# Optimization experiments

Hardware: AMD Instinct MI355X
Metric: run time of the kernel (lower is better)

The kernel has to match this reference:

```python
import jax, jax.numpy as jnp
import numpy as np

N_NODES = 307
U = 100          # gru units / GAT out dim
D_IN = 3         # per-node input features
F_IN = U + D_IN  # 103, GATv2 input dim
NEG_SLOPE = 0.2


def setup_inputs() -> dict:
    key = jax.random.key(0)
    ks = jax.random.split(key, 12)
    B, E = 256, 4096
    inputs = jax.random.normal(ks[0], (B, N_NODES * D_IN), dtype=jnp.float32)
    state = jax.random.normal(ks[1], (B, N_NODES * U), dtype=jnp.float32)
    src = jax.random.randint(ks[2], (E,), 0, N_NODES, dtype=jnp.int32)
    dst = jax.random.randint(ks[3], (E,), 0, N_NODES, dtype=jnp.int32)
    def glorot(k, shape):
        lim = float(np.sqrt(6.0 / (shape[0] + shape[1])))
        return jax.random.uniform(k, shape, jnp.float32, -lim, lim)
    return {
        "inputs": inputs, "state": state, "src": src, "dst": dst,
        "Wl": glorot(ks[4], (F_IN, U)),        # GATv2 lin_l (source)
        "Wr": glorot(ks[5], (F_IN, U)),        # GATv2 lin_r (target)
        "att": jax.random.normal(ks[6], (U,), jnp.float32) * 0.1,
        "gat_bias": jnp.zeros((U,), jnp.float32),
        "bias_gc": jnp.zeros((U,), jnp.float32),   # self.bias_1 added in _gc3
        "W_gru1": glorot(ks[7], (F_IN, 2 * U)),    # GRULinear(100,200)
        "b_gru1": jnp.zeros((2 * U,), jnp.float32),
        "W_gru2": glorot(ks[8], (F_IN, U)),        # GRULinear(100,100)
        "b_gru2": jnp.zeros((U,), jnp.float32),
    }


def _gru_linear(inputs, hidden, W, b):
    # cat((inputs[B,N,3], hidden[B,N,U]), -1) @ W + b
    B = hidden.shape[0]
    x = jnp.concatenate([inputs.reshape(B, N_NODES, D_IN),
                         hidden.reshape(B, N_NODES, U)], axis=2)
    return jnp.einsum('bnf,fo->bno', x, W) + b


def _gatv2(x, src, dst, Wl, Wr, att, gat_bias):
    # x: (B, N, F_IN); PyG GATv2Conv with heads=1, add_self_loops=True
    loops = jnp.arange(N_NODES, dtype=src.dtype)
    s = jnp.concatenate([src, loops])
    d = jnp.concatenate([dst, loops])
    xl = jnp.einsum('bnf,fu->bnu', x, Wl)  # source transform
    xr = jnp.einsum('bnf,fu->bnu', x, Wr)  # target transform

    def per_sample(xl_b, xr_b):
        m = xl_b[s]                                        # (E', U)
        e = jax.nn.leaky_relu(m + xr_b[d], NEG_SLOPE) @ att  # (E',)
        emax = jax.ops.segment_max(e, d, num_segments=N_NODES)
        ex = jnp.exp(e - emax[d])
        denom = jax.ops.segment_sum(ex, d, num_segments=N_NODES)
        alpha = ex / denom[d]
        return jax.ops.segment_sum(alpha[:, None] * m, d, num_segments=N_NODES)

    out = jax.vmap(per_sample)(xl, xr)  # (B, N, U)
    return out + gat_bias


def reference(inputs, state, src, dst, Wl, Wr, att, gat_bias, bias_gc,
              W_gru1, b_gru1, W_gru2, b_gru2):
    B = state.shape[0]
    # _gc3: cat([state, inputs]) -> GATv2 per sample -> + bias_1
    x = jnp.concatenate([state.reshape(B, N_NODES, U),
                         inputs.reshape(B, N_NODES, D_IN)], axis=2)
    st = _gatv2(x, src, dst, Wl, Wr, att, gat_bias) + bias_gc
    st = st.reshape(B, N_NODES * U)
    # GRU gating
    value = jax.nn.sigmoid(_gru_linear(inputs, st, W_gru1, b_gru1))  # (B,N,2U)
    r, u = jnp.split(value, 2, axis=-1)
    r = r.reshape(B, N_NODES * U)
    u = u.reshape(B, N_NODES * U)
    c = jnp.tanh(_gru_linear(inputs, r * st, W_gru2, b_gru2)).reshape(B, N_NODES * U)
    return u * st + (1.0 - u) * c
```

## Files before the change

kernel.cpp:

```cpp
#include <hip/hip_runtime.h>
#include <math.h>

#define NN 307
#define UU 100
#define DD 3
#define UP 104
#define UNIT_W 14336
#define SC_CAP 4608
#define EI_CAP 4416
#define NTILE 20
#define NT 512

typedef _Float16 f16;
typedef f16  f16x2 __attribute__((ext_vector_type(2)));
typedef f16  f16x4 __attribute__((ext_vector_type(4)));
typedef f16  f16x8 __attribute__((ext_vector_type(8)));
typedef float f32x4 __attribute__((ext_vector_type(4)));
typedef unsigned short u16;

__global__ __launch_bounds__(256)
void pack_w_k(const float* __restrict__ Wl, const float* __restrict__ Wr,
              const float* __restrict__ Wg1, const float* __restrict__ Wg2,
              f16* __restrict__ Wp)
{
    const int idx = blockIdx.x * 256 + threadIdx.x;
    const int u   = idx / UNIT_W;
    const int rem = idx - u * UNIT_W;
    const int e   = rem & 7;
    const int l   = (rem >> 3) & 63;
    const int sj  = rem >> 9;
    const int s   = sj / 7, j = sj - 7 * s;
    const int col = j * 16 + (l & 15);
    const int k   = (s * 4 + (l >> 4)) * 8 + e;
    float v = 0.f;
    if (col < UU && k < UU + DD) {
        if (u == 0)      v = Wl[k * UU + col];
        else if (u == 1) v = Wr[k * UU + col];
        else {
            const int kk = (k < UU) ? (k + DD) : (k - UU);
            if (u == 2)      v = Wg1[kk * (2 * UU) + col];
            else if (u == 3) v = Wg1[kk * (2 * UU) + UU + col];
            else             v = Wg2[kk * UU + col];
        }
    }
    Wp[idx] = (f16)v;
}

__global__ __launch_bounds__(64)
void csr_count_k(const int* __restrict__ dst, int E, int* offs)
{
    const int d = blockIdx.x;
    const int lane = threadIdx.x;
    const int Etot = E + NN;
    int c = 0;
    for (int base = 0; base < Etot; base += 64) {
        const int e = base + lane;
        if (e < Etot) {
            const int de = (e < E) ? dst[e] : (e - E);
            c += (de == d) ? 1 : 0;
        }
    }
    #pragma unroll
    for (int m = 1; m < 64; m <<= 1) c += __shfl_xor(c, m, 64);
    if (lane == 0) {
        offs[d + 1] = c;
        if (d == 0) offs[0] = 0;
    }
}

__global__ __launch_bounds__(512)
void csr_scan_k(int* offs)
{
    __shared__ int c[512];
    const int t = threadIdx.x;
    c[t] = (t < NN) ? offs[t + 1] : 0;
    __syncthreads();
    #pragma unroll
    for (int off = 1; off < 512; off <<= 1) {
        const int v = (t >= off) ? c[t - off] : 0;
        __syncthreads();
        c[t] += v;
        __syncthreads();
    }
    if (t < NN) offs[t + 1] = c[t];
    if (t == 0) offs[0] = 0;
}

__global__ __launch_bounds__(64)
void csr_fill_k(const int* __restrict__ src, const int* __restrict__ dst,
                int E, const int* __restrict__ offs,
                int* eidx, int* ddst)
{
    const int d = blockIdx.x;
    const int lane = threadIdx.x;
    const int Etot = E + NN;
    int w = offs[d];
    for (int base = 0; base < Etot; base += 64) {
        const int e = base + lane;
        bool match = false;
        int se = 0;
        if (e < Etot) {
            const int de = (e < E) ? dst[e] : (e - E);
            se           = (e < E) ? src[e] : (e - E);
            match = (de == d);
        }
        const unsigned long long mask = __ballot(match);
        if (match) {
            const int pos = w + __popcll(mask & ((1ULL << lane) - 1ULL));
            eidx[pos] = se;
            ddst[pos] = d;
        }
        w += __popcll(mask);
    }
}

__device__ __forceinline__ void mma_unit1(const f16x8 (&af)[4],
                                          const f16* __restrict__ Wu,
                                          int l, f32x4 (&acc)[7])
{
    #pragma unroll
    for (int s = 0; s < 4; ++s) {
        #pragma unroll
        for (int j = 0; j < 7; ++j) {
            const f16x8 bv = *(const f16x8*)(Wu + (((s * 7 + j) * 64 + l) << 3));
            acc[j] = __builtin_amdgcn_mfma_f32_16x16x32_f16(af[s], bv, acc[j], 0, 0, 0);
        }
        __builtin_amdgcn_sched_barrier(0);
    }
}

__device__ __forceinline__ void z7(f32x4 (&acc)[7])
{
    #pragma unroll
    for (int j = 0; j < 7; ++j) acc[j] = (f32x4)0.f;
}

__global__ __launch_bounds__(NT)
__attribute__((amdgpu_waves_per_eu(2)))
void gat_all_k(const float* __restrict__ state, const float* __restrict__ inputs,
               const f16* __restrict__ Wp, const float* __restrict__ att,
               const float* __restrict__ gb, const float* __restrict__ bgc,
               const int* __restrict__ offs, const int* __restrict__ eidx,
               const int* __restrict__ ddst, int Etot,
               f16* __restrict__ stg)
{
    __shared__ f16   xl_s[NN * UP];
    __shared__ f16   xr_s[NN * UP];
    __shared__ float sc_s[SC_CAP];
    __shared__ u16   ei_s[EI_CAP];
    __shared__ f16   att_s[UP];

    const int b   = blockIdx.x;
    const int tid = threadIdx.x;
    const int w = tid >> 6, l = tid & 63, lr = l & 15, lk = l >> 4;
    const float* stf = state  + (size_t)b * NN * UU;
    const float* inb = inputs + (size_t)b * NN * DD;
    f16* stb = stg + (size_t)b * NN * UP;

    for (int q = tid; q < Etot; q += NT) ei_s[q] = (u16)eidx[q];
    for (int q = tid; q < 2 * NN; q += NT) {
        const int rr = (q < NN) ? q : (q - NN);
        f16* p = (q < NN) ? xl_s : xr_s;
        *(f16x4*)&p[rr * UP + 100] = (f16x4)(f16)0.f;
    }
    if (tid < UP) att_s[tid] = (tid < UU) ? (f16)att[tid] : (f16)0.f;

    for (int tile = w; tile < NTILE; tile += 8) {
        const int row  = tile * 16 + lr;
        const int crow = (row < NN) ? row : (NN - 1);
        const float* bf = stf + (size_t)crow * UU;
        f16x8 af[4];
        #pragma unroll
        for (int s = 0; s < 3; ++s) {
            const int kb = s * 4 + lk;
            const float4 x0 = *(const float4*)(bf + kb * 8);
            const float4 x1 = *(const float4*)(bf + kb * 8 + 4);
            f16x8 v;
            v[0]=(f16)x0.x; v[1]=(f16)x0.y; v[2]=(f16)x0.z; v[3]=(f16)x0.w;
            v[4]=(f16)x1.x; v[5]=(f16)x1.y; v[6]=(f16)x1.z; v[7]=(f16)x1.w;
            af[s] = v;
        }
        {
            f16x8 v = (f16x8)(f16)0.f;
            if (lk == 0) {
                const float4 x0 = *(const float4*)(bf + 96);
                v[0]=(f16)x0.x; v[1]=(f16)x0.y; v[2]=(f16)x0.z; v[3]=(f16)x0.w;
                v[4] = (f16)inb[(size_t)crow * DD + 0];
                v[5] = (f16)inb[(size_t)crow * DD + 1];
                v[6] = (f16)inb[(size_t)crow * DD + 2];
                v[7] = (f16)0.f;
            }
            af[3] = v;
        }
        __builtin_amdgcn_sched_barrier(0);
        #pragma unroll
        for (int u = 0; u < 2; ++u) {
            f32x4 acc[7];
            z7(acc);
            mma_unit1(af, Wp + (size_t)u * UNIT_W, l, acc);
            f16* dst = u ? xr_s : xl_s;
            #pragma unroll
            for (int j = 0; j < 7; ++j) {
                const int col = j * 16 + lr;
                if (col >= UU) continue;
                #pragma unroll
                for (int r = 0; r < 4; ++r) {
                    const int grow = tile * 16 + lk * 4 + r;
                    if (grow < NN) dst[grow * UP + col] = (f16)acc[j][r];
                }
            }
        }
    }
    __syncthreads();

    for (int i = tid; i < Etot; i += NT) {
        const int s = ei_s[i];
        const int d = ddst[i];
        const f16x8* a8 = (const f16x8*)&xl_s[s * UP];
        const f16x8* r8 = (const f16x8*)&xr_s[d * UP];
        float p0 = 0.f, p1 = 0.f;
        #pragma clang loop unroll(disable)
        for (int c = 0; c < 13; ++c) {
            const f16x8 x  = a8[c] + r8[c];
            const f16x8 xm = x * (f16)0.2f;
            const f16x8 y  = __builtin_elementwise_max(x, xm);
            const f16x2* y2  = (const f16x2*)&y;
            const f16x2* at2 = (const f16x2*)&att_s[c * 8];
#if __has_builtin(__builtin_amdgcn_fdot2)
            p0 = __builtin_amdgcn_fdot2(y2[0], at2[0], p0, false);
            p1 = __builtin_amdgcn_fdot2(y2[1], at2[1], p1, false);
            p0 = __builtin_amdgcn_fdot2(y2[2], at2[2], p0, false);
            p1 = __builtin_amdgcn_fdot2(y2[3], at2[3], p1, false);
#else
            #pragma unroll
            for (int q = 0; q < 4; ++q) {
                p0 += (float)y2[q][0] * (float)at2[q][0];
                p1 += (float)y2[q][1] * (float)at2[q][1];
            }
#endif
        }
        sc_s[i] = p0 + p1;
    }
    __syncthreads();

    if (tid < NN) {
        const int e0 = offs[tid], e1 = offs[tid + 1];
        float mx = -1e30f;
        for (int e = e0; e < e1; ++e) mx = fmaxf(mx, sc_s[e]);
        float dn = 0.f;
        for (int e = e0; e < e1; ++e) {
            const float ex = __expf(sc_s[e] - mx);
            sc_s[e] = ex;
            dn += ex;
        }
        const float inv = 1.f / dn;
        for (int e = e0; e < e1; ++e) sc_s[e] *= inv;
    }
    __syncthreads();

    {
        const int g   = tid >> 4;
        const int sub = tid & 15;
        const bool fa = (sub < 13);
        float bias_r[8];
        #pragma unroll
        for (int k = 0; k < 8; ++k) {
            const int f = sub * 8 + k;
            bias_r[k] = (fa && f < UU) ? (gb[f] + bgc[f]) : 0.f;
        }
        for (int d = g; d < NN; d += 32) {
            const int e0 = offs[d], e1 = offs[d + 1];
            float acc[8] = {0.f, 0.f, 0.f, 0.f, 0.f, 0.f, 0.f, 0.f};
            for (int e = e0; e < e1; ++e) {
                const float alpha = sc_s[e];
                const int s = ei_s[e];
                if (fa) {
                    const f16x8 m = *(const f16x8*)&xl_s[s * UP + sub * 8];
                    #pragma unroll
                    for (int k = 0; k < 8; ++k) acc[k] += alpha * (float)m[k];
                }
            }
            if (fa) {
                f16x8 o;
                #pragma unroll
                for (int k = 0; k < 8; ++k) o[k] = (f16)(acc[k] + bias_r[k]);
                *(f16x8*)(stb + (size_t)d * UP + sub * 8) = o;
            }
        }
    }
}

__global__ __launch_bounds__(256, 4)
void gru3_k(const f16* __restrict__ st, const float* __restrict__ inp,
            const f16* __restrict__ Wp2 ,
            const float* __restrict__ bg1, const float* __restrict__ bg2,
            float* __restrict__ out, int M)
{
    __shared__ f16 st_s[64 * UP];
    __shared__ f16 rst_s[64 * UP];

    const int tid = threadIdx.x;
    const int w = tid >> 6, l = tid & 63, lr = l & 15, lk = l >> 4;
    const int rb = blockIdx.x * 64 + w * 16;
    const int lbase = w * 16;

    #pragma unroll
    for (int p = 0; p < 4; ++p) {
        const int idx = p * 64 + l;
        const int row = idx >> 4, ch = idx & 15;
        if (ch < 13) {
            int gr = rb + row; if (gr >= M) gr = M - 1;
            *(f16x8*)&st_s[(lbase + row) * UP + ch * 8] =
                *(const f16x8*)(st + (size_t)gr * UP + ch * 8);
        }
    }

    int crow = rb + lr; if (crow >= M) crow = M - 1;
    const f16* bh = &st_s[(lbase + lr) * UP];
    f16x8 af[4];
    #pragma unroll
    for (int s = 0; s < 3; ++s)
        af[s] = *(const f16x8*)(bh + (s * 4 + lk) * 8);
    {
        f16x8 v = (f16x8)(f16)0.f;
        if (lk == 0) {
            v = *(const f16x8*)(bh + 96);
            v[4] = (f16)inp[(size_t)crow * DD + 0];
            v[5] = (f16)inp[(size_t)crow * DD + 1];
            v[6] = (f16)inp[(size_t)crow * DD + 2];
            v[7] = (f16)0.f;
        }
        af[3] = v;
    }
    __builtin_amdgcn_sched_barrier(0);

    f32x4 acc[7];

    z7(acc);
    mma_unit1(af, Wp2, l, acc);
    #pragma unroll
    for (int j = 0; j < 7; ++j) {
        const int col = j * 16 + lr;
        if (col >= UU) continue;
        const float bR = bg1[col];
        #pragma unroll
        for (int r = 0; r < 4; ++r) {
            const int grow = rb + lk * 4 + r;
            const int lrow = lbase + lk * 4 + r;
            if (grow < M) {
                const float stv = (float)st_s[lrow * UP + col];
                const float sg = 1.f / (1.f + __expf(-(acc[j][r] + bR)));
                rst_s[lrow * UP + col] = (f16)(sg * stv);
            }
        }
    }
    if (l < 16) {
        const int grow2 = rb + l;
        const int lrow2 = lbase + l;
        if (grow2 < M) {
            rst_s[lrow2 * UP + 100] = (f16)inp[(size_t)grow2 * DD + 0];
            rst_s[lrow2 * UP + 101] = (f16)inp[(size_t)grow2 * DD + 1];
            rst_s[lrow2 * UP + 102] = (f16)inp[(size_t)grow2 * DD + 2];
            rst_s[lrow2 * UP + 103] = (f16)0.f;
        }
    }
    __builtin_amdgcn_sched_barrier(0);

    z7(acc);
    mma_unit1(af, Wp2 + UNIT_W, l, acc);
    f16x4 uh[7];
    #pragma unroll
    for (int j = 0; j < 7; ++j) {
        const int col = j * 16 + lr;
        const float bU = (col < UU) ? bg1[UU + col] : 0.f;
        #pragma unroll
        for (int r = 0; r < 4; ++r)
            uh[j][r] = (f16)(1.f / (1.f + __expf(-(acc[j][r] + bU))));
    }

    f16x8 af2[4];
    #pragma unroll
    for (int s = 0; s < 3; ++s)
        af2[s] = *(const f16x8*)&rst_s[(lbase + lr) * UP + (s * 4 + lk) * 8];
    af2[3] = (lk == 0) ? *(const f16x8*)&rst_s[(lbase + lr) * UP + 96]
                       : (f16x8)(f16)0.f;
    __builtin_amdgcn_sched_barrier(0);

    z7(acc);
    mma_unit1(af2, Wp2 + 2 * UNIT_W, l, acc);
    #pragma unroll
    for (int j = 0; j < 7; ++j) {
        const int col = j * 16 + lr;
        if (col >= UU) continue;
        const float bC = bg2[col];
        #pragma unroll
        for (int r = 0; r < 4; ++r) {
            const int grow = rb + lk * 4 + r;
            const int lrow = lbase + lk * 4 + r;
            if (grow < M) {
                const float c = tanhf(acc[j][r] + bC);
                const float u = (float)uh[j][r];
                const float stv = (float)st_s[lrow * UP + col];
                out[(size_t)grow * UU + col] = u * stv + (1.f - u) * c;
            }
        }
    }
}

extern "C" void kernel_launch(void* const* d_in, const int* in_sizes, int n_in,
                              void* d_out, int out_size, void* d_ws, size_t ws_size,
                              hipStream_t stream)
{
    const float* inputs   = (const float*)d_in[0];
    const float* state    = (const float*)d_in[1];
    const int*   src      = (const int*)  d_in[2];
    const int*   dst      = (const int*)  d_in[3];
    const float* Wl       = (const float*)d_in[4];
    const float* Wr       = (const float*)d_in[5];
    const float* att      = (const float*)d_in[6];
    const float* gat_bias = (const float*)d_in[7];
    const float* bias_gc  = (const float*)d_in[8];
    const float* Wg1      = (const float*)d_in[9];
    const float* bg1      = (const float*)d_in[10];
    const float* Wg2      = (const float*)d_in[11];
    const float* bg2      = (const float*)d_in[12];

    const int E = in_sizes[2];
    const int B = in_sizes[1] / (NN * UU);
    const int M = B * NN;
    const int Etot = E + NN;

    char* ws = (char*)d_ws;
    f16* Wp   = (f16*)ws;
    int* offs = (int*)(ws + 5 * UNIT_W * sizeof(f16));
    int* eidx = offs + (NN + 1);
    int* ddst = eidx + (Etot + 64);
    f16* st_h = (f16*)(ws + (256 << 10));
    float* out = (float*)d_out;

    pack_w_k<<<280, 256, 0, stream>>>(Wl, Wr, Wg1, Wg2, Wp);
    csr_count_k<<<NN, 64, 0, stream>>>(dst, E, offs);
    csr_scan_k<<<1, 512, 0, stream>>>(offs);
    csr_fill_k<<<NN, 64, 0, stream>>>(src, dst, E, offs, eidx, ddst);

    gat_all_k<<<B, NT, 0, stream>>>(state, inputs, Wp, att,
        gat_bias, bias_gc, offs, eidx, ddst, Etot, st_h);

    gru3_k<<<(M + 63) / 64, 256, 0, stream>>>(st_h, inputs,
        Wp + 2 * (size_t)UNIT_W, bg1, bg2, out, M);
}
```

Baseline: 165.0 us.

## Split GAT into separate xl/xr GEMM kernel and lighter-LDS attention kernel

Moves the per-sample xl/xr projection GEMM out of the fused GAT kernel into its own batched GEMM kernel that writes fp16 xl/xr to workspace. The attention kernel then keeps only xl in shared memory, reads xr from global, and packs each edge's source index with an fp16 score/alpha into one 32-bit word. The goal is to cut LDS use so more blocks fit per CU, and to run the GEMM over the whole batch with better occupancy. In exchange it adds an extra global round-trip of xl/xr and stores scores and alphas in fp16, which lowers precision.

```diff
diff --git a/kernel.cpp b/kernel.cpp
--- a/kernel.cpp
+++ b/kernel.cpp
@@ -6,9 +6,7 @@
 #define DD 3
 #define UP 104
 #define UNIT_W 14336
-#define SC_CAP 4608
-#define EI_CAP 4416
-#define NTILE 20
+#define SE_CAP 4416
 #define NT 512
 
 typedef _Float16 f16;
@@ -17,6 +15,9 @@
 typedef f16  f16x8 __attribute__((ext_vector_type(8)));
 typedef float f32x4 __attribute__((ext_vector_type(4)));
 typedef unsigned short u16;
+
+__device__ __forceinline__ u16 f16_bits(f16 v) { u16 r; __builtin_memcpy(&r, &v, 2); return r; }
+__device__ __forceinline__ f16 bits_f16(u16 v) { f16 r; __builtin_memcpy(&r, &v, 2); return r; }
 
 __global__ __launch_bounds__(256)
 void pack_w_k(const float* __restrict__ Wl, const float* __restrict__ Wr,
@@ -135,40 +136,19 @@
     for (int j = 0; j < 7; ++j) acc[j] = (f32x4)0.f;
 }
 
-__global__ __launch_bounds__(NT)
-__attribute__((amdgpu_waves_per_eu(2)))
-void gat_all_k(const float* __restrict__ state, const float* __restrict__ inputs,
-               const f16* __restrict__ Wp, const float* __restrict__ att,
-               const float* __restrict__ gb, const float* __restrict__ bgc,
-               const int* __restrict__ offs, const int* __restrict__ eidx,
-               const int* __restrict__ ddst, int Etot,
-               f16* __restrict__ stg)
-{
-    __shared__ f16   xl_s[NN * UP];
-    __shared__ f16   xr_s[NN * UP];
-    __shared__ float sc_s[SC_CAP];
-    __shared__ u16   ei_s[EI_CAP];
-    __shared__ f16   att_s[UP];
-
-    const int b   = blockIdx.x;
+__global__ __launch_bounds__(256, 4)
+void gemm_xlxr_k(const float* __restrict__ state, const float* __restrict__ inp,
+                 const f16* __restrict__ Wp,
+                 f16* __restrict__ xl, f16* __restrict__ xr, int M)
+{
     const int tid = threadIdx.x;
     const int w = tid >> 6, l = tid & 63, lr = l & 15, lk = l >> 4;
-    const float* stf = state  + (size_t)b * NN * UU;
-    const float* inb = inputs + (size_t)b * NN * DD;
-    f16* stb = stg + (size_t)b * NN * UP;
-
-    for (int q = tid; q < Etot; q += NT) ei_s[q] = (u16)eidx[q];
-    for (int q = tid; q < 2 * NN; q += NT) {
-        const int rr = (q < NN) ? q : (q - NN);
-        f16* p = (q < NN) ? xl_s : xr_s;
-        *(f16x4*)&p[rr * UP + 100] = (f16x4)(f16)0.f;
-    }
-    if (tid < UP) att_s[tid] = (tid < UU) ? (f16)att[tid] : (f16)0.f;
-
-    for (int tile = w; tile < NTILE; tile += 8) {
-        const int row  = tile * 16 + lr;
-        const int crow = (row < NN) ? row : (NN - 1);
-        const float* bf = stf + (size_t)crow * UU;
+
+    #pragma clang loop unroll(disable)
+    for (int t = 0; t < 2; ++t) {
+        const int rb = blockIdx.x * 128 + w * 32 + t * 16;
+        int crow = rb + lr; if (crow >= M) crow = M - 1;
+        const float* bf = state + (size_t)crow * UU;
         f16x8 af[4];
         #pragma unroll
         for (int s = 0; s < 3; ++s) {
@@ -185,9 +165,9 @@
             if (lk == 0) {
                 const float4 x0 = *(const float4*)(bf + 96);
                 v[0]=(f16)x0.x; v[1]=(f16)x0.y; v[2]=(f16)x0.z; v[3]=(f16)x0.w;
-                v[4] = (f16)inb[(size_t)crow * DD + 0];
-                v[5] = (f16)inb[(size_t)crow * DD + 1];
-                v[6] = (f16)inb[(size_t)crow * DD + 2];
+                v[4] = (f16)inp[(size_t)crow * DD + 0];
+                v[5] = (f16)inp[(size_t)crow * DD + 1];
+                v[6] = (f16)inp[(size_t)crow * DD + 2];
                 v[7] = (f16)0.f;
             }
             af[3] = v;
@@ -198,26 +178,49 @@
             f32x4 acc[7];
             z7(acc);
             mma_unit1(af, Wp + (size_t)u * UNIT_W, l, acc);
-            f16* dst = u ? xr_s : xl_s;
+            f16* dst = u ? xr : xl;
             #pragma unroll
             for (int j = 0; j < 7; ++j) {
                 const int col = j * 16 + lr;
                 if (col >= UU) continue;
                 #pragma unroll
                 for (int r = 0; r < 4; ++r) {
-                    const int grow = tile * 16 + lk * 4 + r;
-                    if (grow < NN) dst[grow * UP + col] = (f16)acc[j][r];
+                    const int row = rb + lk * 4 + r;
+                    if (row < M) dst[(size_t)row * UP + col] = (f16)acc[j][r];
                 }
             }
         }
     }
+}
+
+__global__ __launch_bounds__(NT, 4)
+void gat2_k(const f16* __restrict__ xl, const f16* __restrict__ xr,
+            const int* __restrict__ offs, const int* __restrict__ eidx,
+            const int* __restrict__ ddst,
+            const float* __restrict__ att, const float* __restrict__ gb,
+            const float* __restrict__ bgc, int Etot,
+            f16* __restrict__ stg)
+{
+    __shared__ f16      xl_s[NN * UP];
+    __shared__ unsigned sa_s[SE_CAP];
+    __shared__ f16      att_s[UP];
+
+    const int b   = blockIdx.x;
+    const int tid = threadIdx.x;
+    const f16* xlb = xl + (size_t)b * NN * UP;
+    const f16* xrb = xr + (size_t)b * NN * UP;
+    f16* stb = stg + (size_t)b * NN * UP;
+
+    if (tid < UP) att_s[tid] = (tid < UU) ? (f16)att[tid] : (f16)0.f;
+    for (int c = tid; c < NN * UP / 8; c += NT)
+        *(f16x8*)&xl_s[c * 8] = *(const f16x8*)&xlb[c * 8];
     __syncthreads();
 
     for (int i = tid; i < Etot; i += NT) {
-        const int s = ei_s[i];
+        const int s = eidx[i];
         const int d = ddst[i];
         const f16x8* a8 = (const f16x8*)&xl_s[s * UP];
-        const f16x8* r8 = (const f16x8*)&xr_s[d * UP];
+        const f16x8* r8 = (const f16x8*)(xrb + (size_t)d * UP);
         float p0 = 0.f, p1 = 0.f;
         #pragma clang loop unroll(disable)
         for (int c = 0; c < 13; ++c) {
@@ -239,22 +242,25 @@
             }
 #endif
         }
-        sc_s[i] = p0 + p1;
+        const f16 ph = (f16)(p0 + p1);
+        sa_s[i] = ((unsigned)s << 16) | (unsigned)f16_bits(ph);
     }
     __syncthreads();
 
     if (tid < NN) {
         const int e0 = offs[tid], e1 = offs[tid + 1];
         float mx = -1e30f;
-        for (int e = e0; e < e1; ++e) mx = fmaxf(mx, sc_s[e]);
+        for (int e = e0; e < e1; ++e)
+            mx = fmaxf(mx, (float)bits_f16((u16)sa_s[e]));
         float dn = 0.f;
+        for (int e = e0; e < e1; ++e)
+            dn += __expf((float)bits_f16((u16)sa_s[e]) - mx);
+        const float inv = 1.f / dn;
         for (int e = e0; e < e1; ++e) {
-            const float ex = __expf(sc_s[e] - mx);
-            sc_s[e] = ex;
-            dn += ex;
-        }
-        const float inv = 1.f / dn;
-        for (int e = e0; e < e1; ++e) sc_s[e] *= inv;
+            const unsigned v = sa_s[e];
+            const f16 al = (f16)(__expf((float)bits_f16((u16)v) - mx) * inv);
+            sa_s[e] = (v & 0xFFFF0000u) | (unsigned)f16_bits(al);
+        }
     }
     __syncthreads();
 
@@ -272,8 +278,9 @@
             const int e0 = offs[d], e1 = offs[d + 1];
             float acc[8] = {0.f, 0.f, 0.f, 0.f, 0.f, 0.f, 0.f, 0.f};
             for (int e = e0; e < e1; ++e) {
-                const float alpha = sc_s[e];
-                const int s = ei_s[e];
+                const unsigned v = sa_s[e];
+                const float alpha = (float)bits_f16((u16)v);
+                const int s = (int)(v >> 16);
                 if (fa) {
                     const f16x8 m = *(const f16x8*)&xl_s[s * UP + sub * 8];
                     #pragma unroll
@@ -435,7 +442,9 @@
     int* offs = (int*)(ws + 5 * UNIT_W * sizeof(f16));
     int* eidx = offs + (NN + 1);
     int* ddst = eidx + (Etot + 64);
-    f16* st_h = (f16*)(ws + (256 << 10));
+    f16* xl_h = (f16*)(ws + (256 << 10));
+    f16* xr_h = xl_h + (size_t)M * UP;
+    f16* st_h = xr_h + (size_t)M * UP;
     float* out = (float*)d_out;
 
     pack_w_k<<<280, 256, 0, stream>>>(Wl, Wr, Wg1, Wg2, Wp);
@@ -443,8 +452,11 @@
     csr_scan_k<<<1, 512, 0, stream>>>(offs);
     csr_fill_k<<<NN, 64, 0, stream>>>(src, dst, E, offs, eidx, ddst);
 
-    gat_all_k<<<B, NT, 0, stream>>>(state, inputs, Wp, att,
-        gat_bias, bias_gc, offs, eidx, ddst, Etot, st_h);
+    gemm_xlxr_k<<<(M + 127) / 128, 256, 0, stream>>>(state, inputs, Wp,
+                                                     xl_h, xr_h, M);
+
+    gat2_k<<<B, NT, 0, stream>>>(xl_h, xr_h, offs, eidx, ddst,
+                                 att, gat_bias, bias_gc, Etot, st_h);
 
     gru3_k<<<(M + 63) / 64, 256, 0, stream>>>(st_h, inputs,
         Wp + 2 * (size_t)UNIT_W, bg1, bg2, out, M);
```

After: 231.6 us. +40.4%, slower.
